# Optimization experiments

Hardware: AMD Instinct MI355X
Metric: run time of the kernel (lower is better)

The kernel has to match this reference:

```python
import jax, jax.numpy as jnp
import numpy as np

N, E, D = 50000, 800000, 64


def _gru_cell(inp, h, w_ih, w_hh, b_ih, b_hh):
    # torch.nn.GRUCell semantics; gates ordered (r, z, n)
    gi = inp @ w_ih.T + b_ih            # [N, 3D]
    gh = h @ w_hh.T + b_hh              # [N, 3D]
    i_r, i_z, i_n = jnp.split(gi, 3, axis=-1)
    h_r, h_z, h_n = jnp.split(gh, 3, axis=-1)
    r = jax.nn.sigmoid(i_r + h_r)
    z = jax.nn.sigmoid(i_z + h_z)
    n = jnp.tanh(i_n + r * h_n)
    return (1.0 - z) * n + z * h


def _dcgru(x, edge_index, edge_weight, w_ih, w_hh, b_ih, b_hh):
    src, dst = edge_index[0], edge_index[1]
    # gather neighbor features, weight by edge, scatter-add to targets
    msg = x[src] * edge_weight                       # [E, D]
    aggr = jax.ops.segment_sum(msg, dst, num_segments=N)  # [N, D]
    return _gru_cell(aggr, x, w_ih, w_hh, b_ih, b_hh)


def setup_inputs() -> dict:
    key = jax.random.key(0)
    ks = jax.random.split(key, 11)
    s = 1.0 / np.sqrt(D)
    inp = {
        'x': jax.random.normal(ks[0], (N, D), jnp.float32),
        'edge_index': jax.random.randint(ks[1], (2, E), 0, N, jnp.int64),
        'edge_weight': jax.random.uniform(ks[2], (E, 1), jnp.float32),
        'w_ih1': jax.random.uniform(ks[3], (3 * D, D), jnp.float32, -s, s),
        'w_hh1': jax.random.uniform(ks[4], (3 * D, D), jnp.float32, -s, s),
        'b_ih1': jax.random.uniform(ks[5], (3 * D,), jnp.float32, -s, s),
        'b_hh1': jax.random.uniform(ks[6], (3 * D,), jnp.float32, -s, s),
        'w_ih2': jax.random.uniform(ks[7], (3 * D, D), jnp.float32, -s, s),
        'w_hh2': jax.random.uniform(ks[8], (3 * D, D), jnp.float32, -s, s),
        'b_ih2': jax.random.uniform(ks[9], (3 * D,), jnp.float32, -s, s),
        'b_hh2': jax.random.uniform(ks[10], (3 * D,), jnp.float32, -s, s),
    }
    return inp


def reference(x, edge_index, edge_weight, w_ih1, w_hh1, b_ih1, b_hh1,
              w_ih2, w_hh2, b_ih2, b_hh2):
    h = _dcgru(x, edge_index, edge_weight, w_ih1, w_hh1, b_ih1, b_hh1)
    out = _dcgru(h, edge_index, edge_weight, w_ih2, w_hh2, b_ih2, b_hh2)
    return out
```

## Files before the change

### kernel.cpp

```cpp
#include <hip/hip_runtime.h>

#define NN 50000
#define NE 800000
#define DD 64
#define NT (NN / 16)
#define NBUK 1024
#define BUCKN 49
#define EBLK 4096
#define NBBIN 196
#define SCN (NBUK * NBBIN)
#define NSB 784
#define CONVB 3173

typedef float     f32x4 __attribute__((ext_vector_type(4)));
typedef _Float16  f16x8 __attribute__((ext_vector_type(8)));
typedef _Float16  f16x4 __attribute__((ext_vector_type(4)));

union h2u { _Float16 f; unsigned short u; };

__global__ void prep_kernel(const float* __restrict__ x,
                            const float* __restrict__ w0, const float* __restrict__ w1,
                            const float* __restrict__ w2, const float* __restrict__ w3,
                            _Float16* __restrict__ xh, _Float16* __restrict__ wh,
                            const int* __restrict__ ei, unsigned* __restrict__ SC) {
    if (blockIdx.x < CONVB) {
        int i = blockIdx.x * 256 + threadIdx.x;
        const int XQ = NN * DD / 4;
        if (i < XQ) {
            float4 v = ((const float4*)x)[i];
            f16x4 o = { (_Float16)v.x, (_Float16)v.y, (_Float16)v.z, (_Float16)v.w };
            ((f16x4*)xh)[i] = o;
        } else {
            int wi = i - XQ;
            if (wi >= 4 * 3072) return;
            int mat = wi / 3072, q = wi - mat * 3072;
            const float* s = mat == 0 ? w0 : mat == 1 ? w1 : mat == 2 ? w2 : w3;
            float4 v = ((const float4*)s)[q];
            f16x4 o = { (_Float16)v.x, (_Float16)v.y, (_Float16)v.z, (_Float16)v.w };
            ((f16x4*)(wh + mat * 12288))[q] = o;
        }
    } else {
        int blk = blockIdx.x - CONVB;
        __shared__ unsigned lcnt[NBUK];
        for (int i = threadIdx.x; i < NBUK; i += 256) lcnt[i] = 0;
        __syncthreads();
        int base = blk * EBLK;
        int lim = NE - base; if (lim > EBLK) lim = EBLK;
        for (int k = threadIdx.x; k < lim; k += 256) {
            unsigned dst = (unsigned)ei[NE + base + k];
            atomicAdd(&lcnt[dst / BUCKN], 1u);
        }
        __syncthreads();
        for (int i = threadIdx.x; i < NBUK; i += 256)
            SC[i * NBBIN + blk] = lcnt[i];
    }
}

__global__ void scan1_kernel(const unsigned* __restrict__ SC, unsigned* __restrict__ psum) {
    __shared__ unsigned red[256];
    int i = blockIdx.x * 256 + threadIdx.x;
    red[threadIdx.x] = SC[i];
    __syncthreads();
    for (int d = 128; d > 0; d >>= 1) {
        if (threadIdx.x < d) red[threadIdx.x] += red[threadIdx.x + d];
        __syncthreads();
    }
    if (threadIdx.x == 0) psum[blockIdx.x] = red[0];
}

__global__ void scan2_kernel(unsigned* __restrict__ psum) {
    __shared__ unsigned tmp[256];
    int t = threadIdx.x;
    unsigned running = 0;
    for (int c = 0; c < (NSB + 255) / 256; ++c) {
        int i = c * 256 + t;
        unsigned v = (i < NSB) ? psum[i] : 0;
        tmp[t] = v;
        __syncthreads();
        #pragma unroll
        for (int d = 1; d < 256; d <<= 1) {
            unsigned add = (t >= d) ? tmp[t - d] : 0;
            __syncthreads();
            tmp[t] += add;
            __syncthreads();
        }
        if (i < NSB) psum[i] = running + tmp[t] - v;
        unsigned tot = tmp[255];
        __syncthreads();
        running += tot;
    }
}

__global__ void scan3_kernel(unsigned* __restrict__ SC, const unsigned* __restrict__ psum) {
    __shared__ unsigned tmp[256];
    int t = threadIdx.x;
    int i = blockIdx.x * 256 + t;
    unsigned v = SC[i];
    tmp[t] = v;
    __syncthreads();
    #pragma unroll
    for (int d = 1; d < 256; d <<= 1) {
        unsigned add = (t >= d) ? tmp[t - d] : 0;
        __syncthreads();
        tmp[t] += add;
        __syncthreads();
    }
    SC[i] = psum[blockIdx.x] + tmp[t] - v;
}

__global__ __launch_bounds__(256) void place_kernel(const int* __restrict__ ei,
                                                    const float* __restrict__ ew,
                                                    const unsigned* __restrict__ SC,
                                                    unsigned* __restrict__ sp,
                                                    _Float16* __restrict__ sw) {
    __shared__ unsigned lbase[NBUK];
    __shared__ unsigned lcur[NBUK];
    int blk = blockIdx.x;
    for (int i = threadIdx.x; i < NBUK; i += 256) {
        lbase[i] = SC[i * NBBIN + blk];
        lcur[i] = 0;
    }
    __syncthreads();
    int base = blk * EBLK;
    int lim = NE - base; if (lim > EBLK) lim = EBLK;
    for (int k = threadIdx.x; k < lim; k += 256) {
        int e = base + k;
        unsigned dst = (unsigned)ei[NE + e];
        unsigned buk = dst / BUCKN;
        unsigned dl  = dst - buk * BUCKN;
        unsigned r = atomicAdd(&lcur[buk], 1u);
        unsigned pos = lbase[buk] + r;
        sp[pos] = (unsigned)ei[e] | (dl << 16);
        sw[pos] = (_Float16)ew[e];
    }
}

__global__ __launch_bounds__(256) void sort2_kernel(const unsigned* __restrict__ SC,
                                                    const unsigned* __restrict__ sp,
                                                    const _Float16* __restrict__ sw,
                                                    unsigned* __restrict__ pw,
                                                    int* __restrict__ off) {
    __shared__ unsigned hist[BUCKN], nbase[BUCKN], cur[BUCKN];
    int b = blockIdx.x;
    unsigned start = SC[b * NBBIN];
    unsigned end   = (b + 1 < NBUK) ? SC[(b + 1) * NBBIN] : NE;
    int cnt = (int)(end - start);
    if (threadIdx.x < BUCKN) { hist[threadIdx.x] = 0; cur[threadIdx.x] = 0; }
    __syncthreads();
    for (int k = threadIdx.x; k < cnt; k += 256)
        atomicAdd(&hist[sp[start + k] >> 16], 1u);
    __syncthreads();
    if (threadIdx.x == 0) {
        unsigned run = 0;
        for (int i = 0; i < BUCKN; ++i) { nbase[i] = run; run += hist[i]; }
    }
    __syncthreads();
    if (threadIdx.x < BUCKN)
        off[b * BUCKN + threadIdx.x] = (int)(start + nbase[threadIdx.x]);
    for (int k = threadIdx.x; k < cnt; k += 256) {
        unsigned v = sp[start + k];
        unsigned dl = v >> 16;
        unsigned r = atomicAdd(&cur[dl], 1u);
        h2u c; c.f = sw[start + k];
        pw[start + nbase[dl] + r] = (v & 0xFFFFu) | ((unsigned)c.u << 16);
    }
}

__global__ __launch_bounds__(256) void aggr_kernel(const int* __restrict__ off,
                                                   const unsigned* __restrict__ pw,
                                                   const _Float16* __restrict__ xh,
                                                   _Float16* __restrict__ aggrh) {
    int wv = (blockIdx.x * 256 + threadIdx.x) >> 6;
    if (wv >= NN) return;
    int lane = threadIdx.x & 63;
    int s = off[wv], e = off[wv + 1];
    int n = e - s;
    const unsigned* p = pw + s;
    float acc = 0.f;
    for (int i = 0; i < n; i += 8) {
        unsigned P[8];
        #pragma unroll
        for (int j = 0; j < 8; ++j) {
            int idx = (i + j < n) ? i + j : n - 1;
            P[j] = p[idx];
        }
        float a[8], w[8];
        #pragma unroll
        for (int j = 0; j < 8; ++j) a[j] = (float)xh[(P[j] & 0xFFFFu) * DD + lane];
        #pragma unroll
        for (int j = 0; j < 8; ++j) {
            h2u c; c.u = (unsigned short)(P[j] >> 16);
            w[j] = (i + j < n) ? (float)c.f : 0.f;
        }
        #pragma unroll
        for (int j = 0; j < 8; ++j) acc += a[j] * w[j];
    }
    aggrh[wv * DD + lane] = (_Float16)acc;
}

__global__ __launch_bounds__(256) void gru_kernel(
    const _Float16* __restrict__ aggrh,
    const _Float16* __restrict__ hA,
    const _Float16* __restrict__ wih,
    const _Float16* __restrict__ whh,
    const float* __restrict__ bih, const float* __restrict__ bhh,
    float* __restrict__ outF,
    _Float16* __restrict__ outH)
{
    __shared__ _Float16 W[2 * 192 * 72];
    #pragma unroll
    for (int it = 0; it < 12; ++it) {
        int idx = threadIdx.x + it * 256;
        int mat = idx >= 1536 ? 1 : 0;
        int lid = idx - mat * 1536;
        int o = lid >> 3, k8 = (lid & 7) << 3;
        f16x8 v = *(const f16x8*)((mat ? whh : wih) + o * 64 + k8);
        *(f16x8*)&W[mat * 13824 + o * 72 + k8] = v;
    }
    __syncthreads();

    int lane = threadIdx.x & 63;
    int tile = blockIdx.x * 4 + (threadIdx.x >> 6);
    if (tile >= NT) return;
    int base = tile << 4;
    int c = lane & 15, g = lane >> 4;

    f16x8 Aa[2], Ah[2];
    {
        const _Float16* ap = aggrh + (base + c) * DD + g * 8;
        const _Float16* hp = hA    + (base + c) * DD + g * 8;
        #pragma unroll
        for (int s = 0; s < 2; ++s) {
            Aa[s] = *(const f16x8*)(ap + s * 32);
            Ah[s] = *(const f16x8*)(hp + s * 32);
        }
    }

    f32x4 acc[12], hn[4];
    #pragma unroll
    for (int t = 0; t < 12; ++t) acc[t] = f32x4{0.f, 0.f, 0.f, 0.f};
    #pragma unroll
    for (int t = 0; t < 4; ++t) hn[t] = f32x4{0.f, 0.f, 0.f, 0.f};

    #pragma unroll
    for (int t = 0; t < 12; ++t) {
        #pragma unroll
        for (int s = 0; s < 2; ++s) {
            f16x8 b = *(const f16x8*)&W[(t * 16 + c) * 72 + s * 32 + g * 8];
            acc[t] = __builtin_amdgcn_mfma_f32_16x16x32_f16(Aa[s], b, acc[t], 0, 0, 0);
        }
    }
    #pragma unroll
    for (int t = 0; t < 8; ++t) {
        #pragma unroll
        for (int s = 0; s < 2; ++s) {
            f16x8 b = *(const f16x8*)&W[13824 + (t * 16 + c) * 72 + s * 32 + g * 8];
            acc[t] = __builtin_amdgcn_mfma_f32_16x16x32_f16(Ah[s], b, acc[t], 0, 0, 0);
        }
    }
    #pragma unroll
    for (int t = 0; t < 4; ++t) {
        #pragma unroll
        for (int s = 0; s < 2; ++s) {
            f16x8 b = *(const f16x8*)&W[13824 + ((t + 8) * 16 + c) * 72 + s * 32 + g * 8];
            hn[t] = __builtin_amdgcn_mfma_f32_16x16x32_f16(Ah[s], b, hn[t], 0, 0, 0);
        }
    }

    float br[4], bz[4], bi_[4], bh_[4];
    #pragma unroll
    for (int j = 0; j < 4; ++j) {
        int d = j * 16 + c;
        br[j] = bih[d] + bhh[d];
        bz[j] = bih[64 + d] + bhh[64 + d];
        bi_[j] = bih[128 + d];
        bh_[j] = bhh[128 + d];
    }

    #pragma unroll
    for (int m = 0; m < 4; ++m) {
        int n = base + g * 4 + m;
        #pragma unroll
        for (int j = 0; j < 4; ++j) {
            int d = j * 16 + c;
            float rv = 1.f / (1.f + __expf(-(acc[j][m] + br[j])));
            float zv = 1.f / (1.f + __expf(-(acc[4 + j][m] + bz[j])));
            float nv = tanhf(acc[8 + j][m] + bi_[j] + rv * (hn[j][m] + bh_[j]));
            float hold = (float)hA[n * DD + d];
            float o = (1.f - zv) * nv + zv * hold;
            if (outF) outF[n * DD + d] = o;
            else      outH[n * DD + d] = (_Float16)o;
        }
    }
}

extern "C" void kernel_launch(void* const* d_in, const int* in_sizes, int n_in,
                              void* d_out, int out_size, void* d_ws, size_t ws_size,
                              hipStream_t stream) {
    const float* x    = (const float*)d_in[0];
    const int*   ei   = (const int*)d_in[1];
    const float* ew   = (const float*)d_in[2];
    const float* wih1 = (const float*)d_in[3];
    const float* whh1 = (const float*)d_in[4];
    const float* bih1 = (const float*)d_in[5];
    const float* bhh1 = (const float*)d_in[6];
    const float* wih2 = (const float*)d_in[7];
    const float* whh2 = (const float*)d_in[8];
    const float* bih2 = (const float*)d_in[9];
    const float* bhh2 = (const float*)d_in[10];
    float* out = (float*)d_out;

    char* ws = (char*)d_ws;
    _Float16* xh    = (_Float16*)ws;
    _Float16* h1h   = (_Float16*)(ws + 6400000);
    unsigned* pw    = (unsigned*)(ws + 12800000);
    unsigned* sp    = (unsigned*)(ws + 16000000);
    _Float16* sw    = (_Float16*)(ws + 19200000);
    unsigned* SC    = (unsigned*)(ws + 20800000);
    unsigned* psum  = (unsigned*)(ws + 21602816);
    _Float16* aggrh = (_Float16*)(ws + 16000000);
    _Float16* wh    = (_Float16*)(ws + 22400000);
    int*      off   = (int*)     (ws + 22498304);

    prep_kernel<<<CONVB + NBBIN, 256, 0, stream>>>(x, wih1, whh1, wih2, whh2,
                                                   xh, wh, ei, SC);
    scan1_kernel<<<NSB, 256, 0, stream>>>(SC, psum);
    scan2_kernel<<<1, 256, 0, stream>>>(psum);
    scan3_kernel<<<NSB, 256, 0, stream>>>(SC, psum);
    place_kernel<<<NBBIN, 256, 0, stream>>>(ei, ew, SC, sp, sw);
    sort2_kernel<<<NBUK, 256, 0, stream>>>(SC, sp, sw, pw, off);

    aggr_kernel<<<NN * 64 / 256, 256, 0, stream>>>(off, pw, xh, aggrh);
    gru_kernel<<<(NT + 3) / 4, 256, 0, stream>>>(aggrh, xh,
                                                 wh, wh + 12288, bih1, bhh1,
                                                 nullptr, h1h);

    aggr_kernel<<<NN * 64 / 256, 256, 0, stream>>>(off, pw, h1h, aggrh);
    gru_kernel<<<(NT + 3) / 4, 256, 0, stream>>>(aggrh, h1h,
                                                 wh + 2 * 12288, wh + 3 * 12288, bih2, bhh2,
                                                 out, nullptr);
}
```

Before: 132.1 us.

## Replace three-kernel scan with single-pass decoupled look-back scan

Merges the reduce, scan-of-partials and downsweep kernels into one scan kernel that uses decoupled look-back over a flag and value status array. The status array is zeroed inside the prep kernel. This removes two kernel launches and a serial single-block pass. The cost is spin-waiting on predecessor blocks, which relies on blocks being scheduled in order and on relaxed atomics being visible to other blocks.

New measurement: 130.6 us. About the same (-1.2%).

```diff
diff --git a/kernel.cpp b/kernel.cpp
--- a/kernel.cpp
+++ b/kernel.cpp
@@ -22,7 +22,8 @@
                             const float* __restrict__ w0, const float* __restrict__ w1,
                             const float* __restrict__ w2, const float* __restrict__ w3,
                             _Float16* __restrict__ xh, _Float16* __restrict__ wh,
-                            const int* __restrict__ ei, unsigned* __restrict__ SC) {
+                            const int* __restrict__ ei, unsigned* __restrict__ SC,
+                            unsigned long long* __restrict__ st) {
     if (blockIdx.x < CONVB) {
         int i = blockIdx.x * 256 + threadIdx.x;
         const int XQ = NN * DD / 4;
@@ -42,6 +43,8 @@
     } else {
         int blk = blockIdx.x - CONVB;
         __shared__ unsigned lcnt[NBUK];
+        if (blk == 0)
+            for (int i = threadIdx.x; i < NSB; i += 256) st[i] = 0ull;
         for (int i = threadIdx.x; i < NBUK; i += 256) lcnt[i] = 0;
         __syncthreads();
         int base = blk * EBLK;
@@ -56,56 +59,69 @@
     }
 }
 
-__global__ void scan1_kernel(const unsigned* __restrict__ SC, unsigned* __restrict__ psum) {
-    __shared__ unsigned red[256];
-    int i = blockIdx.x * 256 + threadIdx.x;
-    red[threadIdx.x] = SC[i];
-    __syncthreads();
-    for (int d = 128; d > 0; d >>= 1) {
-        if (threadIdx.x < d) red[threadIdx.x] += red[threadIdx.x + d];
-        __syncthreads();
-    }
-    if (threadIdx.x == 0) psum[blockIdx.x] = red[0];
-}
-
-__global__ void scan2_kernel(unsigned* __restrict__ psum) {
-    __shared__ unsigned tmp[256];
-    int t = threadIdx.x;
-    unsigned running = 0;
-    for (int c = 0; c < (NSB + 255) / 256; ++c) {
-        int i = c * 256 + t;
-        unsigned v = (i < NSB) ? psum[i] : 0;
-        tmp[t] = v;
-        __syncthreads();
-        #pragma unroll
-        for (int d = 1; d < 256; d <<= 1) {
-            unsigned add = (t >= d) ? tmp[t - d] : 0;
-            __syncthreads();
-            tmp[t] += add;
-            __syncthreads();
-        }
-        if (i < NSB) psum[i] = running + tmp[t] - v;
-        unsigned tot = tmp[255];
-        __syncthreads();
-        running += tot;
-    }
-}
-
-__global__ void scan3_kernel(unsigned* __restrict__ SC, const unsigned* __restrict__ psum) {
-    __shared__ unsigned tmp[256];
-    int t = threadIdx.x;
-    int i = blockIdx.x * 256 + t;
+__global__ __launch_bounds__(256) void scan_kernel(unsigned* __restrict__ SC,
+                                                   unsigned long long* __restrict__ st) {
+    __shared__ unsigned lds[256];
+    __shared__ unsigned s_exc;
+    int b = blockIdx.x, t = threadIdx.x;
+    int i = b * 256 + t;
     unsigned v = SC[i];
-    tmp[t] = v;
+    lds[t] = v;
     __syncthreads();
     #pragma unroll
     for (int d = 1; d < 256; d <<= 1) {
-        unsigned add = (t >= d) ? tmp[t - d] : 0;
-        __syncthreads();
-        tmp[t] += add;
-        __syncthreads();
-    }
-    SC[i] = psum[blockIdx.x] + tmp[t] - v;
+        unsigned add = (t >= d) ? lds[t - d] : 0;
+        __syncthreads();
+        lds[t] += add;
+        __syncthreads();
+    }
+    unsigned aggregate = lds[255];
+    if (t == 0) {
+        unsigned long long val = (b == 0) ? ((2ull << 32) | aggregate)
+                                          : ((1ull << 32) | aggregate);
+        __atomic_store_n(&st[b], val, __ATOMIC_RELAXED);
+    }
+    if (b > 0) {
+        if (t < 64) {
+            unsigned run = 0;
+            int p = b - 1;
+            for (;;) {
+                int idx = p - t;
+                unsigned f, val;
+                unsigned long long m2, m0;
+                int l2;
+                for (;;) {
+                    if (idx >= 0) {
+                        unsigned long long w =
+                            __atomic_load_n(&st[idx], __ATOMIC_RELAXED);
+                        f = (unsigned)(w >> 32);
+                        val = (unsigned)w;
+                    } else { f = 2u; val = 0u; }
+                    m2 = __ballot(f == 2u);
+                    m0 = __ballot(f == 0u);
+                    l2 = (m2 != 0ull) ? (__ffsll((long long)m2) - 1) : 64;
+                    unsigned long long below =
+                        (l2 >= 64) ? ~0ull : ((1ull << l2) - 1ull);
+                    if ((m0 & below) == 0ull) break;
+                }
+                unsigned contrib = (t <= l2 && idx >= 0) ? val : 0u;
+                #pragma unroll
+                for (int s = 32; s > 0; s >>= 1)
+                    contrib += __shfl_xor(contrib, s, 64);
+                run += contrib;
+                if (l2 < 64) break;
+                p -= 64;
+            }
+            if (t == 0) {
+                s_exc = run;
+                __atomic_store_n(&st[b], (2ull << 32) | (run + aggregate),
+                                 __ATOMIC_RELAXED);
+            }
+        }
+        __syncthreads();
+    }
+    unsigned exc = (b == 0) ? 0u : s_exc;
+    SC[i] = exc + lds[t] - v;
 }
 
 __global__ __launch_bounds__(256) void place_kernel(const int* __restrict__ ei,
@@ -317,16 +333,14 @@
     unsigned* sp    = (unsigned*)(ws + 16000000);
     _Float16* sw    = (_Float16*)(ws + 19200000);
     unsigned* SC    = (unsigned*)(ws + 20800000);
-    unsigned* psum  = (unsigned*)(ws + 21602816);
+    unsigned long long* st = (unsigned long long*)(ws + 21602816);
     _Float16* aggrh = (_Float16*)(ws + 16000000);
     _Float16* wh    = (_Float16*)(ws + 22400000);
     int*      off   = (int*)     (ws + 22498304);
 
     prep_kernel<<<CONVB + NBBIN, 256, 0, stream>>>(x, wih1, whh1, wih2, whh2,
-                                                   xh, wh, ei, SC);
-    scan1_kernel<<<NSB, 256, 0, stream>>>(SC, psum);
-    scan2_kernel<<<1, 256, 0, stream>>>(psum);
-    scan3_kernel<<<NSB, 256, 0, stream>>>(SC, psum);
+                                                   xh, wh, ei, SC, st);
+    scan_kernel<<<NSB, 256, 0, stream>>>(SC, st);
     place_kernel<<<NBBIN, 256, 0, stream>>>(ei, ew, SC, sp, sw);
     sort2_kernel<<<NBUK, 256, 0, stream>>>(SC, sp, sw, pw, off);
 
```
